# Optimization experiments

Hardware: AMD Instinct MI355X
Metric: run time of the kernel (lower is better)

Reference implementation:

```python
import jax, jax.numpy as jnp
import numpy as np

DIM = 512
HEADS = 6
DH = 64
INNER = HEADS * DH  # 384
M = 20              # num_landmarks
PINV_ITERS = 6
KERNEL = 33         # residual_conv_kernel
SCALE = DH ** -0.5


def setup_inputs() -> dict:
    key = jax.random.key(0)
    ks = jax.random.split(key, 7)
    x = jax.random.normal(ks[0], (16, 6000, DIM), dtype=jnp.float32)
    norm_w = jnp.ones((DIM,), dtype=jnp.float32)
    norm_b = jnp.zeros((DIM,), dtype=jnp.float32)
    w_qkv = jax.random.normal(ks[1], (DIM, 3 * INNER), dtype=jnp.float32) * 0.02
    w_out = jax.random.normal(ks[2], (INNER, DIM), dtype=jnp.float32) * 0.02
    b_out = jnp.zeros((DIM,), dtype=jnp.float32)
    # depthwise conv over seq dim: torch Conv2d(heads, heads, (33,1), groups=heads)
    res_kernel = jax.random.normal(ks[3], (HEADS, 1, KERNEL, 1), dtype=jnp.float32) * 0.1
    return {"x": x, "norm_w": norm_w, "norm_b": norm_b, "w_qkv": w_qkv,
            "w_out": w_out, "b_out": b_out, "res_kernel": res_kernel}


def moore_penrose_pinv(a, iters=PINV_ITERS):
    # a: [b, h, m, m]
    abs_a = jnp.abs(a)
    denom = abs_a.sum(-1).max() * abs_a.sum(-2).max()  # global maxes, as in torch ref
    z = jnp.swapaxes(a, -1, -2) / denom
    I = jnp.eye(a.shape[-1], dtype=a.dtype)
    for _ in range(iters):
        az = a @ z
        z = 0.25 * z @ (13.0 * I - az @ (15.0 * I - az @ (7.0 * I - az)))
    return z


def nystrom_attention(xn, w_qkv, w_out, b_out, res_kernel):
    b, n, _ = xn.shape
    qkv = xn @ w_qkv  # [b, n, 3*inner]
    q, k, v = jnp.split(qkv, 3, axis=-1)
    to_heads = lambda t: t.reshape(b, n, HEADS, DH).transpose(0, 2, 1, 3)  # b h n d
    q, k, v = to_heads(q), to_heads(k), to_heads(v)
    q = q * SCALE

    l = n // M  # n chosen as multiple of m, so no padding branch
    q_land = q.reshape(b, HEADS, M, l, DH).mean(axis=3)  # b h m d
    k_land = k.reshape(b, HEADS, M, l, DH).mean(axis=3)

    sim1 = jnp.einsum('bhid,bhjd->bhij', q, k_land)       # b h n m
    sim2 = jnp.einsum('bhid,bhjd->bhij', q_land, k_land)  # b h m m
    sim3 = jnp.einsum('bhid,bhjd->bhij', q_land, k)       # b h m n

    attn1 = jax.nn.softmax(sim1, axis=-1)
    attn2 = jax.nn.softmax(sim2, axis=-1)
    attn3 = jax.nn.softmax(sim3, axis=-1)

    attn2_inv = moore_penrose_pinv(attn2)
    out = (attn1 @ attn2_inv) @ (attn3 @ v)  # b h n d

    # residual depthwise conv along seq dim, per head (groups=heads)
    pad = KERNEL // 2
    conv = jax.lax.conv_general_dilated(
        v, res_kernel, window_strides=(1, 1), padding=((pad, pad), (0, 0)),
        dimension_numbers=('NCHW', 'OIHW', 'NCHW'), feature_group_count=HEADS)
    out = out + conv

    out = out.transpose(0, 2, 1, 3).reshape(b, n, INNER)
    return out @ w_out + b_out


def reference(x, norm_w, norm_b, w_qkv, w_out, b_out, res_kernel):
    mu = x.mean(-1, keepdims=True)
    var = jnp.mean((x - mu) ** 2, axis=-1, keepdims=True)
    xn = (x - mu) / jnp.sqrt(var + 1e-5) * norm_w + norm_b
    return x + nystrom_attention(xn, w_qkv, w_out, b_out, res_kernel)
```

## Files before the change

### kernel.cpp

```cpp
#include <hip/hip_runtime.h>

typedef float  f32x4  __attribute__((ext_vector_type(4)));
typedef __bf16 bf16x4 __attribute__((ext_vector_type(4)));
typedef __bf16 bf16x8 __attribute__((ext_vector_type(8)));

#define B_     16
#define N_     6000
#define D_     512
#define H_     6
#define DH_    64
#define INNER_ 384
#define M_     20
#define L_     300
#define KW_    33
#define ROWS_  (B_ * N_)
#define SCALE_ 0.125f
#define CH2_   128
#define NCH2_  47

__device__ __forceinline__ ushort f2bf(float f) {
    __bf16 h = (__bf16)f;
    return __builtin_bit_cast(ushort, h);
}
__device__ __forceinline__ float bf2f(ushort h) {
    return __uint_as_float(((unsigned)h) << 16);
}

#define GLD(gp, lp) __builtin_amdgcn_global_load_lds( \
    (const __attribute__((address_space(1))) unsigned int*)(gp), \
    (__attribute__((address_space(3))) unsigned int*)(lp), 16, 0, 0)

__global__ __launch_bounds__(256) void ln_kernel(const float* __restrict__ x,
        const float* __restrict__ w, const float* __restrict__ b,
        ushort* __restrict__ xn) {
    int row  = blockIdx.x * 4 + (threadIdx.x >> 6);
    int lane = threadIdx.x & 63;
    const float4* xp = (const float4*)(x + (size_t)row * D_);
    float4 v0 = xp[lane];
    float4 v1 = xp[lane + 64];
    float s  = v0.x + v0.y + v0.z + v0.w + v1.x + v1.y + v1.z + v1.w;
    float sq = v0.x*v0.x + v0.y*v0.y + v0.z*v0.z + v0.w*v0.w
             + v1.x*v1.x + v1.y*v1.y + v1.z*v1.z + v1.w*v1.w;
    #pragma unroll
    for (int o = 32; o; o >>= 1) { s += __shfl_xor(s, o); sq += __shfl_xor(sq, o); }
    float mu   = s * (1.0f / D_);
    float var  = sq * (1.0f / D_) - mu * mu;
    float rstd = rsqrtf(var + 1e-5f);
    const float4 wv0 = ((const float4*)w)[lane];
    const float4 wv1 = ((const float4*)w)[lane + 64];
    const float4 bv0 = ((const float4*)b)[lane];
    const float4 bv1 = ((const float4*)b)[lane + 64];
    ushort4 o0, o1;
    o0.x = f2bf((v0.x - mu) * rstd * wv0.x + bv0.x);
    o0.y = f2bf((v0.y - mu) * rstd * wv0.y + bv0.y);
    o0.z = f2bf((v0.z - mu) * rstd * wv0.z + bv0.z);
    o0.w = f2bf((v0.w - mu) * rstd * wv0.w + bv0.w);
    o1.x = f2bf((v1.x - mu) * rstd * wv1.x + bv1.x);
    o1.y = f2bf((v1.y - mu) * rstd * wv1.y + bv1.y);
    o1.z = f2bf((v1.z - mu) * rstd * wv1.z + bv1.z);
    o1.w = f2bf((v1.w - mu) * rstd * wv1.w + bv1.w);
    ((ushort4*)(xn + (size_t)row * D_))[lane]      = o0;
    ((ushort4*)(xn + (size_t)row * D_))[lane + 64] = o1;
}

__global__ void transpose_cast_kernel(const float* __restrict__ W, ushort* __restrict__ WT,
                                      int R, int C) {
    int idx = blockIdx.x * blockDim.x + threadIdx.x;
    if (idx >= R * C) return;
    int r = idx / C, c = idx - r * C;
    WT[(size_t)c * R + r] = f2bf(W[idx]);
}

template<int KDIM, int NT, int EPI>
__global__ __launch_bounds__(256) void gemm_kernel(
        const ushort* __restrict__ A, const ushort* __restrict__ BT,
        ushort* __restrict__ qo, ushort* __restrict__ ko, ushort* __restrict__ vo,
        float* __restrict__ outp, const float* __restrict__ xres, const float* __restrict__ bout) {
    __shared__ __align__(16) ushort As[128 * 32];
    __shared__ __align__(16) ushort Bs[128 * 32];

    const int nwg = (int)gridDim.x;
    const int orig = (int)blockIdx.x;
    const int qd = nwg >> 3, rm = nwg & 7;
    const int xcd = orig & 7, loc = orig >> 3;
    const int wg = (xcd < rm ? xcd * (qd + 1) : rm * (qd + 1) + (xcd - rm) * qd) + loc;
    const int m0 = (wg / NT) * 128, n0 = (wg % NT) * 128;

    const int tid = threadIdx.x;
    const int lane = tid & 63, wave = tid >> 6;
    const int wm = (wave >> 1) * 64, wn = (wave & 1) * 64;
    const int fr = lane & 15;

    const int seg0 = wave * 2, seg1 = wave * 2 + 1;
    const int srow0 = seg0 * 16 + (lane >> 2);
    const int srow1 = seg1 * 16 + (lane >> 2);
    const int scol  = ((((lane & 3) - ((lane >> 3) & 3)) & 3) * 8);
    const ushort* Ag0 = A  + (size_t)(m0 + srow0) * KDIM + scol;
    const ushort* Ag1 = A  + (size_t)(m0 + srow1) * KDIM + scol;
    const ushort* Bg0 = BT + (size_t)(n0 + srow0) * KDIM + scol;
    const ushort* Bg1 = BT + (size_t)(n0 + srow1) * KDIM + scol;
    ushort* Al0 = &As[seg0 * 512];
    ushort* Al1 = &As[seg1 * 512];
    ushort* Bl0 = &Bs[seg0 * 512];
    ushort* Bl1 = &Bs[seg1 * 512];

    const int rp = (((lane >> 4) + (fr >> 1)) & 3) * 8;

    f32x4 acc[4][4] = {};

    for (int k0 = 0; k0 < KDIM; k0 += 32) {
        __syncthreads();
        GLD(Ag0 + k0, Al0);
        GLD(Ag1 + k0, Al1);
        GLD(Bg0 + k0, Bl0);
        GLD(Bg1 + k0, Bl1);
        __syncthreads();
        bf16x8 af[4], bfv[4];
        #pragma unroll
        for (int i = 0; i < 4; ++i) {
            af[i]  = *(const bf16x8*)&As[(wm + i * 16 + fr) * 32 + rp];
            bfv[i] = *(const bf16x8*)&Bs[(wn + i * 16 + fr) * 32 + rp];
        }
        #pragma unroll
        for (int i = 0; i < 4; ++i)
            #pragma unroll
            for (int j = 0; j < 4; ++j)
                acc[i][j] = __builtin_amdgcn_mfma_f32_16x16x32_bf16(af[i], bfv[j], acc[i][j], 0, 0, 0);
    }

    #pragma unroll
    for (int i = 0; i < 4; ++i) {
        #pragma unroll
        for (int j = 0; j < 4; ++j) {
            #pragma unroll
            for (int rg = 0; rg < 4; ++rg) {
                int gr = m0 + wm + i * 16 + ((lane >> 4) << 2) + rg;
                int gc = n0 + wn + j * 16 + (lane & 15);
                float val = acc[i][j][rg];
                if (EPI == 0) {
                    int bb = gr / N_, ii = gr - bb * N_;
                    int part = gc / INNER_, rem = gc - part * INNER_;
                    int h = rem >> 6, d = rem & 63;
                    size_t di = (((size_t)bb * H_ + h) * N_ + ii) * DH_ + d;
                    if (part == 0)      qo[di] = f2bf(val * SCALE_);
                    else if (part == 1) ko[di] = f2bf(val);
                    else                vo[di] = f2bf(val);
                } else {
                    size_t oi = (size_t)gr * D_ + gc;
                    outp[oi] = val + bout[gc] + xres[oi];
                }
            }
        }
    }
}

__global__ __launch_bounds__(64) void landmark_kernel(const ushort* __restrict__ q,
        const ushort* __restrict__ k, float* __restrict__ qland, float* __restrict__ kland) {
    int bhm = blockIdx.x;
    int bh = bhm / M_, m = bhm - bh * M_;
    const ushort* src = (blockIdx.y == 0) ? q : k;
    float* dst = (blockIdx.y == 0) ? qland : kland;
    int d = threadIdx.x;
    const ushort* p = src + ((size_t)bh * N_ + m * L_) * DH_ + d;
    float s = 0.f;
    #pragma unroll 4
    for (int j = 0; j < L_; ++j) s += bf2f(p[(size_t)j * DH_]);
    dst[((size_t)bh * M_ + m) * DH_ + d] = s * (1.0f / L_);
}

__global__ __launch_bounds__(512) void attn2_kernel(const float* __restrict__ qland,
        const float* __restrict__ kland, float* __restrict__ attn2, unsigned* __restrict__ gmax) {
    int bh = blockIdx.x;
    __shared__ float sim[M_ * M_];
    int t = threadIdx.x;
    if (t < M_ * M_) {
        int i = t / M_, j = t - (t / M_) * M_;
        const float* qp = qland + ((size_t)bh * M_ + i) * DH_;
        const float* kp = kland + ((size_t)bh * M_ + j) * DH_;
        float s = 0.f;
        for (int d = 0; d < DH_; ++d) s += qp[d] * kp[d];
        sim[t] = s;
    }
    __syncthreads();
    if (t < M_) {
        float mx = -1e30f;
        for (int j = 0; j < M_; ++j) mx = fmaxf(mx, sim[t * M_ + j]);
        float s = 0.f;
        for (int j = 0; j < M_; ++j) { float e = __expf(sim[t * M_ + j] - mx); sim[t * M_ + j] = e; s += e; }
        float inv = 1.0f / s;
        for (int j = 0; j < M_; ++j) sim[t * M_ + j] *= inv;
    }
    __syncthreads();
    if (t < M_ * M_) attn2[(size_t)bh * 400 + t] = sim[t];
    if (t < M_) {
        float cs = 0.f, rs = 0.f;
        for (int i = 0; i < M_; ++i) { cs += sim[i * M_ + t]; rs += sim[t * M_ + i]; }
        atomicMax(&gmax[1], __float_as_uint(cs));
        atomicMax(&gmax[0], __float_as_uint(rs));
    }
}

__global__ __launch_bounds__(512) void pinv_kernel(const float* __restrict__ attn2,
        const unsigned* __restrict__ gmax, float* __restrict__ ainv) {
    int bh = blockIdx.x;
    __shared__ float buf[5 * 400];
    float* pa = buf; float* pz = buf + 400; float* m1 = buf + 800; float* m2 = buf + 1200; float* m3 = buf + 1600;
    int t = threadIdx.x;
    float rden = 1.0f / (__uint_as_float(gmax[0]) * __uint_as_float(gmax[1]));
    int i = t / M_, j = t - (t / M_) * M_;
    if (t < 400) {
        pa[t] = attn2[(size_t)bh * 400 + t];
        pz[t] = attn2[(size_t)bh * 400 + j * M_ + i] * rden;
    }
    for (int it = 0; it < 6; ++it) {
        __syncthreads();
        if (t < 400) { float s = 0; for (int kk = 0; kk < M_; ++kk) s += pa[i * M_ + kk] * pz[kk * M_ + j]; m1[t] = s; }
        __syncthreads();
        if (t < 400) { float s = 0; for (int kk = 0; kk < M_; ++kk) s += m1[i * M_ + kk] * m1[kk * M_ + j]; m2[t] = 7.0f * m1[t] - s; }
        __syncthreads();
        if (t < 400) { float s = 0; for (int kk = 0; kk < M_; ++kk) s += m1[i * M_ + kk] * m2[kk * M_ + j]; m3[t] = 15.0f * m1[t] - s; }
        __syncthreads();
        if (t < 400) { float s = 0; for (int kk = 0; kk < M_; ++kk) s += pz[i * M_ + kk] * m3[kk * M_ + j]; m2[t] = 0.25f * (13.0f * pz[t] - s); }
        __syncthreads();
        float* tmp = pz; pz = m2; m2 = tmp;
    }
    if (t < 400) ainv[(size_t)bh * 400 + t] = pz[t];
}

__global__ __launch_bounds__(256) void attn3v_mfma_kernel(
        const float* __restrict__ qland, const ushort* __restrict__ k,
        const ushort* __restrict__ v, float* __restrict__ pacc, float* __restrict__ pden) {
    int ch = blockIdx.x, bh = blockIdx.y;
    __shared__ __align__(16) ushort Ks[CH2_ * 64];
    __shared__ __align__(16) ushort Vs[CH2_ * 64];
    __shared__ __align__(16) ushort qlb[32 * 64];
    __shared__ __align__(16) ushort Pt[32 * 136];
    int t = threadIdx.x;
    int lane = t & 63, wave = t >> 6;
    int j0 = ch * CH2_;
    int jmax = N_ - j0; if (jmax > CH2_) jmax = CH2_;

    const ushort* kbase = k + ((size_t)bh * N_ + j0) * DH_;
    const ushort* vbase = v + ((size_t)bh * N_ + j0) * DH_;
    #pragma unroll
    for (int i = 0; i < 4; ++i) {
        int pdx = (wave * 4 + i) * 64 + lane;
        int row = pdx >> 3, pp = pdx & 7;
        int c = (pp - (row & 7)) & 7;
        int rowc = row < jmax ? row : jmax - 1;
        GLD(kbase + (size_t)rowc * DH_ + c * 8, &Ks[pdx * 8]);
        GLD(vbase + (size_t)rowc * DH_ + c * 8, &Vs[pdx * 8]);
    }
    {
        int row = t >> 3, pp = t & 7;
        int c = (pp - (row & 7)) & 7;
        ushort w8[8];
        if (row < M_) {
            const float* qp = qland + ((size_t)bh * M_ + row) * DH_ + c * 8;
            #pragma unroll
            for (int e = 0; e < 8; ++e) w8[e] = f2bf(qp[e]);
        } else {
            #pragma unroll
            for (int e = 0; e < 8; ++e) w8[e] = 0;
        }
        *(uint4*)&qlb[t * 8] = *(const uint4*)w8;
    }
    __syncthreads();

    int fr = lane & 15, g = lane >> 4;

    f32x4 sacc[2][2] = {};
    #pragma unroll
    for (int ks = 0; ks < 2; ++ks) {
        bf16x8 bq[2];
        #pragma unroll
        for (int mt = 0; mt < 2; ++mt) {
            int m = mt * 16 + fr;
            int c = ks * 4 + g;
            int pp = (c + (m & 7)) & 7;
            bq[mt] = *(const bf16x8*)&qlb[m * 64 + pp * 8];
        }
        #pragma unroll
        for (int jl = 0; jl < 2; ++jl) {
            int row = (wave * 2 + jl) * 16 + fr;
            int c = ks * 4 + g;
            int pp = (c + (row & 7)) & 7;
            bf16x8 ak = *(const bf16x8*)&Ks[row * 64 + pp * 8];
            #pragma unroll
            for (int mt = 0; mt < 2; ++mt)
                sacc[jl][mt] = __builtin_amdgcn_mfma_f32_16x16x32_bf16(ak, bq[mt], sacc[jl][mt], 0, 0, 0);
        }
    }
    #pragma unroll
    for (int jl = 0; jl < 2; ++jl) {
        #pragma unroll
        for (int mt = 0; mt < 2; ++mt) {
            int m = mt * 16 + fr;
            #pragma unroll
            for (int rg = 0; rg < 4; ++rg) {
                int jloc = (wave * 2 + jl) * 16 + 4 * g + rg;
                float e = __expf(sacc[jl][mt][rg]);
                e = (jloc < jmax) ? e : 0.f;
                int c = jloc >> 3;
                int pp = (c & 8) | ((c + (m & 7)) & 7);
                Pt[m * 136 + pp * 8 + (jloc & 7)] = f2bf(e);
            }
        }
    }
    __syncthreads();

    if (t < M_) {
        float s = 0.f;
        #pragma unroll
        for (int cc = 0; cc < 16; ++cc) {
            bf16x8 pv = *(const bf16x8*)&Pt[t * 136 + cc * 8];
            #pragma unroll
            for (int e = 0; e < 8; ++e) s += (float)pv[e];
        }
        pden[((size_t)bh * NCH2_ + ch) * M_ + t] = s;
    }

    f32x4 oacc[2] = {};
    int d = wave * 16 + fr;
    int cch = d >> 3, drem = d & 7;
    #pragma unroll
    for (int ks = 0; ks < 4; ++ks) {
        ushort bw[8];
        #pragma unroll
        for (int e = 0; e < 8; ++e) {
            int j = ks * 32 + g * 8 + e;
            int pp = (cch + (j & 7)) & 7;
            bw[e] = Vs[j * 64 + pp * 8 + drem];
        }
        bf16x8 bv = *(const bf16x8*)bw;
        #pragma unroll
        for (int mt = 0; mt < 2; ++mt) {
            int m = mt * 16 + fr;
            int c = ks * 4 + g;
            int pp = (c & 8) | ((c + (m & 7)) & 7);
            bf16x8 ap = *(const bf16x8*)&Pt[m * 136 + pp * 8];
            oacc[mt] = __builtin_amdgcn_mfma_f32_16x16x32_bf16(ap, bv, oacc[mt], 0, 0, 0);
        }
    }
    #pragma unroll
    for (int mt = 0; mt < 2; ++mt) {
        #pragma unroll
        for (int rg = 0; rg < 4; ++rg) {
            int m = mt * 16 + 4 * g + rg;
            if (m < M_)
                pacc[(((size_t)bh * NCH2_ + ch) * M_ + m) * DH_ + d] = oacc[mt][rg];
        }
    }
}

__global__ __launch_bounds__(256) void akv_kernel(const float* __restrict__ ainv,
        const float* __restrict__ pacc, const float* __restrict__ pden,
        float* __restrict__ akv) {
    int bh = blockIdx.x;
    __shared__ float kvs[M_ * DH_];
    __shared__ float inv_s[M_ * M_];
    __shared__ float den[M_];
    int t = threadIdx.x;
    for (int i = t; i < M_ * M_; i += 256) inv_s[i] = ainv[(size_t)bh * 400 + i];
    if (t < M_) {
        float s = 0.f;
        for (int c = 0; c < NCH2_; ++c) s += pden[((size_t)bh * NCH2_ + c) * M_ + t];
        den[t] = s;
    }
    __syncthreads();
    for (int idx = t; idx < M_ * DH_; idx += 256) {
        int m = idx >> 6;
        float s = 0.f;
        #pragma unroll 4
        for (int c = 0; c < NCH2_; ++c) s += pacc[((size_t)bh * NCH2_ + c) * M_ * DH_ + idx];
        kvs[idx] = s / den[m];
    }
    __syncthreads();
    for (int idx = t; idx < M_ * DH_; idx += 256) {
        int m = idx >> 6, d = idx & 63;
        float s = 0.f;
        #pragma unroll
        for (int mm = 0; mm < M_; ++mm) s += inv_s[m * M_ + mm] * kvs[mm * DH_ + d];
        akv[(size_t)bh * M_ * DH_ + idx] = s;
    }
}

__global__ __launch_bounds__(256) void out_attn_kernel(const ushort* __restrict__ q,
        const ushort* __restrict__ v, const float* __restrict__ kland,
        const float* __restrict__ akv, const float* __restrict__ resk,
        ushort* __restrict__ att_out) {
    int bh = blockIdx.y;
    int b = bh / H_, h = bh - b * H_;
    int r0 = blockIdx.x * 64;
    __shared__ ushort Vs[96 * 64];
    __shared__ float  Cs[64 * 65];
    __shared__ float  klf[M_ * DH_];
    __shared__ float  akvs[M_ * DH_];
    int t = threadIdx.x;

    const ushort* vbase = v + (size_t)bh * N_ * DH_;
    #pragma unroll
    for (int i = 0; i < 3; ++i) {
        int c2 = t + i * 256;
        int row = c2 >> 3, ch = c2 & 7;
        int gr = r0 - 16 + row;
        uint4 val = make_uint4(0u, 0u, 0u, 0u);
        if (gr >= 0 && gr < N_) val = *(const uint4*)(vbase + (size_t)gr * DH_ + ch * 8);
        *(uint4*)&Vs[row * 64 + ch * 8] = val;
    }
    for (int i = t; i < M_ * DH_; i += 256) {
        klf[i]  = kland[(size_t)bh * M_ * DH_ + i];
        akvs[i] = akv[(size_t)bh * M_ * DH_ + i];
    }
    float kr[KW_];
    #pragma unroll
    for (int tt = 0; tt < KW_; ++tt) kr[tt] = resk[h * KW_ + tt];
    __syncthreads();

    {
        int g = t >> 6, d = t & 63;
        float vv[48];
        #pragma unroll
        for (int j = 0; j < 48; ++j) vv[j] = bf2f(Vs[(g * 16 + j) * 64 + d]);
        #pragma unroll
        for (int rr = 0; rr < 16; ++rr) {
            float s = 0.f;
            #pragma unroll
            for (int tt = 0; tt < KW_; ++tt) s += kr[tt] * vv[rr + tt];
            Cs[(g * 16 + rr) * 65 + d] = s;
        }
    }
    __syncthreads();

    int rr = t >> 2, quad = t & 3;
    int r = r0 + rr;
    bool valid = r < N_;
    int rc = valid ? r : N_ - 1;

    float qf[16];
    const uint4* qp = (const uint4*)(q + ((size_t)bh * N_ + rc) * DH_ + quad * 16);
    #pragma unroll
    for (int c = 0; c < 2; ++c) {
        uint4 u = qp[c];
        qf[c*8+0] = bf2f((ushort)(u.x & 0xFFFF)); qf[c*8+1] = bf2f((ushort)(u.x >> 16));
        qf[c*8+2] = bf2f((ushort)(u.y & 0xFFFF)); qf[c*8+3] = bf2f((ushort)(u.y >> 16));
        qf[c*8+4] = bf2f((ushort)(u.z & 0xFFFF)); qf[c*8+5] = bf2f((ushort)(u.z >> 16));
        qf[c*8+6] = bf2f((ushort)(u.w & 0xFFFF)); qf[c*8+7] = bf2f((ushort)(u.w >> 16));
    }

    float p[M_];
    #pragma unroll
    for (int m = 0; m < M_; ++m) {
        const float* kl = &klf[m * DH_ + quad * 16];
        float s = 0.f;
        #pragma unroll
        for (int dd = 0; dd < 16; ++dd) s += qf[dd] * kl[dd];
        s += __shfl_xor(s, 1);
        s += __shfl_xor(s, 2);
        p[m] = s;
    }
    float mx = -1e30f;
    #pragma unroll
    for (int m = 0; m < M_; ++m) mx = fmaxf(mx, p[m]);
    float ssum = 0.f;
    #pragma unroll
    for (int m = 0; m < M_; ++m) { p[m] = __expf(p[m] - mx); ssum += p[m]; }
    float rinv = 1.0f / ssum;
    #pragma unroll
    for (int m = 0; m < M_; ++m) p[m] *= rinv;

    float out[16];
    #pragma unroll
    for (int dd = 0; dd < 16; ++dd) out[dd] = Cs[rr * 65 + quad * 16 + dd];
    #pragma unroll
    for (int m = 0; m < M_; ++m) {
        float w = p[m];
        const float* av = &akvs[m * DH_ + quad * 16];
        #pragma unroll
        for (int dd = 0; dd < 16; ++dd) out[dd] += w * av[dd];
    }

    if (valid) {
        ushort* op = att_out + ((size_t)(b * N_ + r)) * INNER_ + h * DH_ + quad * 16;
        #pragma unroll
        for (int c = 0; c < 2; ++c) {
            uint4 w4;
            w4.x = (unsigned)f2bf(out[c*8+0]) | ((unsigned)f2bf(out[c*8+1]) << 16);
            w4.y = (unsigned)f2bf(out[c*8+2]) | ((unsigned)f2bf(out[c*8+3]) << 16);
            w4.z = (unsigned)f2bf(out[c*8+4]) | ((unsigned)f2bf(out[c*8+5]) << 16);
            w4.w = (unsigned)f2bf(out[c*8+6]) | ((unsigned)f2bf(out[c*8+7]) << 16);
            ((uint4*)op)[c] = w4;
        }
    }
}

extern "C" void kernel_launch(void* const* d_in, const int* in_sizes, int n_in,
                              void* d_out, int out_size, void* d_ws, size_t ws_size,
                              hipStream_t stream) {
    const float* x      = (const float*)d_in[0];
    const float* norm_w = (const float*)d_in[1];
    const float* norm_b = (const float*)d_in[2];
    const float* w_qkv  = (const float*)d_in[3];
    const float* w_out  = (const float*)d_in[4];
    const float* b_out  = (const float*)d_in[5];
    const float* res_k  = (const float*)d_in[6];

    char* wsp = (char*)d_ws;
    size_t off = 0;
    auto alloc = [&](size_t bytes) -> void* {
        void* p = wsp + off;
        off = (off + bytes + 255) & ~(size_t)255;
        return p;
    };
    ushort* xn    = (ushort*)alloc((size_t)ROWS_ * D_ * 2);
    ushort* qb    = (ushort*)alloc((size_t)B_ * H_ * N_ * DH_ * 2);
    ushort* kb    = (ushort*)alloc((size_t)B_ * H_ * N_ * DH_ * 2);
    ushort* vb    = (ushort*)alloc((size_t)B_ * H_ * N_ * DH_ * 2);
    ushort* wqkvT = (ushort*)alloc((size_t)3 * INNER_ * D_ * 2);
    ushort* woutT = (ushort*)alloc((size_t)D_ * INNER_ * 2);
    float*  qland = (float*)alloc((size_t)B_ * H_ * M_ * DH_ * 4);
    float*  kland = (float*)alloc((size_t)B_ * H_ * M_ * DH_ * 4);
    float*  attn2 = (float*)alloc((size_t)B_ * H_ * 400 * 4);
    float*  ainv  = (float*)alloc((size_t)B_ * H_ * 400 * 4);
    float*  pacc  = (float*)alloc((size_t)B_ * H_ * NCH2_ * M_ * DH_ * 4);
    float*  pden  = (float*)alloc((size_t)B_ * H_ * NCH2_ * M_ * 4);
    float*  akvb  = (float*)alloc((size_t)B_ * H_ * M_ * DH_ * 4);
    unsigned* gmx = (unsigned*)alloc(256);
    ushort* att_out = xn;

    hipMemsetAsync(gmx, 0, 8, stream);

    int tn = 3 * INNER_ * D_;
    transpose_cast_kernel<<<(tn + 255) / 256, 256, 0, stream>>>(w_qkv, wqkvT, D_, 3 * INNER_);
    tn = D_ * INNER_;
    transpose_cast_kernel<<<(tn + 255) / 256, 256, 0, stream>>>(w_out, woutT, INNER_, D_);

    ln_kernel<<<ROWS_ / 4, 256, 0, stream>>>(x, norm_w, norm_b, xn);

    gemm_kernel<D_, 9, 0><<<(ROWS_ / 128) * 9, 256, 0, stream>>>(
        xn, wqkvT, qb, kb, vb, nullptr, nullptr, nullptr);

    landmark_kernel<<<dim3(B_ * H_ * M_, 2), 64, 0, stream>>>(qb, kb, qland, kland);

    attn2_kernel<<<B_ * H_, 512, 0, stream>>>(qland, kland, attn2, gmx);
    pinv_kernel<<<B_ * H_, 512, 0, stream>>>(attn2, gmx, ainv);

    attn3v_mfma_kernel<<<dim3(NCH2_, B_ * H_), 256, 0, stream>>>(qland, kb, vb, pacc, pden);

    akv_kernel<<<B_ * H_, 256, 0, stream>>>(ainv, pacc, pden, akvb);

    out_attn_kernel<<<dim3((N_ + 63) / 64, B_ * H_), 256, 0, stream>>>(
        qb, vb, kland, akvb, res_k, att_out);

    gemm_kernel<INNER_, 4, 1><<<(ROWS_ / 128) * 4, 256, 0, stream>>>(
        att_out, woutT, nullptr, nullptr, nullptr, (float*)d_out, x, b_out);
}
```

Baseline: 610.6 us.

## Triple-buffer GEMM LDS tiles with async global loads and vmcnt waits

```diff
diff --git a/kernel.cpp b/kernel.cpp
--- a/kernel.cpp
+++ b/kernel.cpp
@@ -76,8 +76,8 @@
         const ushort* __restrict__ A, const ushort* __restrict__ BT,
         ushort* __restrict__ qo, ushort* __restrict__ ko, ushort* __restrict__ vo,
         float* __restrict__ outp, const float* __restrict__ xres, const float* __restrict__ bout) {
-    __shared__ __align__(16) ushort As[128 * 32];
-    __shared__ __align__(16) ushort Bs[128 * 32];
+    __shared__ __align__(16) ushort As[3][128 * 32];
+    __shared__ __align__(16) ushort Bs[3][128 * 32];
 
     const int nwg = (int)gridDim.x;
     const int orig = (int)blockIdx.x;
@@ -99,33 +99,52 @@
     const ushort* Ag1 = A  + (size_t)(m0 + srow1) * KDIM + scol;
     const ushort* Bg0 = BT + (size_t)(n0 + srow0) * KDIM + scol;
     const ushort* Bg1 = BT + (size_t)(n0 + srow1) * KDIM + scol;
-    ushort* Al0 = &As[seg0 * 512];
-    ushort* Al1 = &As[seg1 * 512];
-    ushort* Bl0 = &Bs[seg0 * 512];
-    ushort* Bl1 = &Bs[seg1 * 512];
 
     const int rp = (((lane >> 4) + (fr >> 1)) & 3) * 8;
 
     f32x4 acc[4][4] = {};
 
-    for (int k0 = 0; k0 < KDIM; k0 += 32) {
-        __syncthreads();
-        GLD(Ag0 + k0, Al0);
-        GLD(Ag1 + k0, Al1);
-        GLD(Bg0 + k0, Bl0);
-        GLD(Bg1 + k0, Bl1);
-        __syncthreads();
+    auto stage = [&](int bI, int k0) {
+        GLD(Ag0 + k0, &As[bI][seg0 * 512]);
+        GLD(Ag1 + k0, &As[bI][seg1 * 512]);
+        GLD(Bg0 + k0, &Bs[bI][seg0 * 512]);
+        GLD(Bg1 + k0, &Bs[bI][seg1 * 512]);
+    };
+    auto compute = [&](int bI) {
         bf16x8 af[4], bfv[4];
         #pragma unroll
         for (int i = 0; i < 4; ++i) {
-            af[i]  = *(const bf16x8*)&As[(wm + i * 16 + fr) * 32 + rp];
-            bfv[i] = *(const bf16x8*)&Bs[(wn + i * 16 + fr) * 32 + rp];
+            af[i]  = *(const bf16x8*)&As[bI][(wm + i * 16 + fr) * 32 + rp];
+            bfv[i] = *(const bf16x8*)&Bs[bI][(wn + i * 16 + fr) * 32 + rp];
         }
         #pragma unroll
         for (int i = 0; i < 4; ++i)
             #pragma unroll
             for (int j = 0; j < 4; ++j)
                 acc[i][j] = __builtin_amdgcn_mfma_f32_16x16x32_bf16(af[i], bfv[j], acc[i][j], 0, 0, 0);
+    };
+
+    constexpr int NSTEP = KDIM / 32;
+    stage(0, 0);
+    stage(1, 32);
+    asm volatile("s_waitcnt vmcnt(4)" ::: "memory");
+    __builtin_amdgcn_sched_barrier(0);
+    __builtin_amdgcn_s_barrier();
+    __builtin_amdgcn_sched_barrier(0);
+
+    int c0 = 0, c1 = 1, c2 = 2;
+    for (int i = 0; i < NSTEP; ++i) {
+        int kn = (i + 2) * 32;
+        if (kn < KDIM) stage(c2, kn);
+        compute(c0);
+        if (i + 1 < NSTEP) {
+            if (kn < KDIM) { asm volatile("s_waitcnt vmcnt(4)" ::: "memory"); }
+            else           { asm volatile("s_waitcnt vmcnt(0)" ::: "memory"); }
+            __builtin_amdgcn_sched_barrier(0);
+            __builtin_amdgcn_s_barrier();
+            __builtin_amdgcn_sched_barrier(0);
+        }
+        int tmp = c0; c0 = c1; c1 = c2; c2 = tmp;
     }
 
     #pragma unroll
```

Result: no change. 616.0 us (+0.9%).
